# Optimization experiments

Measured on AMD Instinct MI355X. Metric: run time of the kernel, lower is better.

The kernel has to match this reference:

```python
import jax, jax.numpy as jnp
import numpy as np

B, S, N, F_IN = 4, 256, 500, 32
D, L = 64, 2
TEMP = 0.5
EPS = 1e-5

def gelu(x):
    return jax.nn.gelu(x, approximate=False)  # torch default GELU (erf)

def layernorm(h, g, b):
    mu = h.mean(-1, keepdims=True)
    var = ((h - mu) ** 2).mean(-1, keepdims=True)
    return (h - mu) * jax.lax.rsqrt(var + EPS) * g + b

def gru_last(x_seq, Wih, Whh, bih, bhh):
    # x_seq: [B, T, I]; torch nn.GRU gate math, h0 = 0; returns final hidden [B, D]
    xp = jnp.einsum('bti,gi->btg', x_seq, Wih) + bih  # precompute input gates [B, T, 3D]
    d = Whh.shape[1]
    def step(h, xpt):
        gh = h @ Whh.T + bhh
        xr, xz, xn = jnp.split(xpt, 3, axis=-1)
        hr, hz, hn = jnp.split(gh, 3, axis=-1)
        r = jax.nn.sigmoid(xr + hr)
        z = jax.nn.sigmoid(xz + hz)
        n = jnp.tanh(xn + r * hn)
        return (1.0 - z) * n + z * h, None
    h0 = jnp.zeros((x_seq.shape[0], d), x_seq.dtype)
    h, _ = jax.lax.scan(step, h0, xp.transpose(1, 0, 2))
    return h

def forward(x, ip_W, ip_b, from_embed, to_embed, gl_W, gl_b, gl_g, gl_be,
            Wih_s, Whh_s, bih_s, bhh_s, Wih_m, Whh_m, bih_m, bhh_m,
            Wih_l, Whh_l, bih_l, bhh_l, dh_W1, dh_b1, dh_W2, dh_b2):
    # input_proj: Linear + GELU (Dropout is identity in eval)
    x = gelu(jnp.einsum('bsnf,df->bsnd', x, ip_W) + ip_b)  # [B,S,N,D]
    # learned adjacency: softmax over destination nodes
    adj = jax.nn.softmax((from_embed @ to_embed.T) / TEMP, axis=-1)  # [N,N]
    for i in range(gl_W.shape[0]):
        agg = jnp.einsum('bsnd,nm->bsmd', x, adj)
        h = gelu(jnp.einsum('bsnd,ed->bsne', x + agg, gl_W[i]) + gl_b[i])
        x = layernorm(h, gl_g[i], gl_be[i])
    b, s, n, d = x.shape
    x_flat = x.reshape(b, s, n * d)
    h_s = gru_last(x_flat[:, -10:, :], Wih_s, Whh_s, bih_s, bhh_s)
    h_m = gru_last(x_flat[:, -20:, :], Wih_m, Whh_m, bih_m, bhh_m)
    h_l = gru_last(x_flat, Wih_l, Whh_l, bih_l, bhh_l)
    h = jnp.concatenate([h_s, h_m, h_l], axis=-1)  # [B, 3D]
    h = gelu(h @ dh_W1.T + dh_b1)
    return h @ dh_W2.T + dh_b2  # direction logits [B, N]

def setup_inputs():
    key = jax.random.key(0)
    it = iter(jax.random.split(key, 40))
    rn = lambda shape, s=0.02: jax.random.normal(next(it), shape, jnp.float32) * s
    I = N * D
    return {
        'x': jax.random.normal(next(it), (B, S, N, F_IN), jnp.float32),
        'ip_W': rn((D, F_IN)), 'ip_b': jnp.zeros((D,), jnp.float32),
        'from_embed': rn((N, 32), 0.1), 'to_embed': rn((N, 32), 0.1),
        'gl_W': rn((L, D, D)), 'gl_b': jnp.zeros((L, D), jnp.float32),
        'gl_g': jnp.ones((L, D), jnp.float32), 'gl_be': jnp.zeros((L, D), jnp.float32),
        'Wih_s': rn((3 * D, I)), 'Whh_s': rn((3 * D, D)),
        'bih_s': jnp.zeros((3 * D,), jnp.float32), 'bhh_s': jnp.zeros((3 * D,), jnp.float32),
        'Wih_m': rn((3 * D, I)), 'Whh_m': rn((3 * D, D)),
        'bih_m': jnp.zeros((3 * D,), jnp.float32), 'bhh_m': jnp.zeros((3 * D,), jnp.float32),
        'Wih_l': rn((3 * D, I)), 'Whh_l': rn((3 * D, D)),
        'bih_l': jnp.zeros((3 * D,), jnp.float32), 'bhh_l': jnp.zeros((3 * D,), jnp.float32),
        'dh_W1': rn((D, 3 * D)), 'dh_b1': jnp.zeros((D,), jnp.float32),
        'dh_W2': rn((N, D)), 'dh_b2': jnp.zeros((N,), jnp.float32),
    }

def reference(x, ip_W, ip_b, from_embed, to_embed, gl_W, gl_b, gl_g, gl_be,
              Wih_s, Whh_s, bih_s, bhh_s, Wih_m, Whh_m, bih_m, bhh_m,
              Wih_l, Whh_l, bih_l, bhh_l, dh_W1, dh_b1, dh_W2, dh_b2):
    return forward(x, ip_W, ip_b, from_embed, to_embed, gl_W, gl_b, gl_g, gl_be,
                   Wih_s, Whh_s, bih_s, bhh_s, Wih_m, Whh_m, bih_m, bhh_m,
                   Wih_l, Whh_l, bih_l, bhh_l, dh_W1, dh_b1, dh_W2, dh_b2)
```

## Files before the change

### kernel.cpp

```cpp
#include <hip/hip_runtime.h>
#include <math.h>

#define NN 500
#define DD 64
#define NPAD 512
#define COLS 65536
#define BS_TOT 1024
#define I_DIM 32000
#define KS_GRU 40
#define KSL 800

typedef __attribute__((ext_vector_type(8))) short bf16x8;
typedef __attribute__((ext_vector_type(4))) float f32x4;

__device__ __forceinline__ float gelu_f(float x) {
    return 0.5f * x * (1.0f + erff(x * 0.70710678118654752440f));
}

__device__ __forceinline__ unsigned short bf16_rn(float x) {
    unsigned int u = __float_as_uint(x);
    unsigned int r = u + 0x7FFFu + ((u >> 16) & 1u);
    return (unsigned short)(r >> 16);
}
__device__ __forceinline__ float bf16_tof(unsigned short h) {
    return __uint_as_float(((unsigned int)h) << 16);
}
__device__ __forceinline__ unsigned int pack_hl(float x) {
    unsigned short h = bf16_rn(x);
    unsigned short l = bf16_rn(x - bf16_tof(h));
    return (unsigned int)h | ((unsigned int)l << 16);
}
__device__ __forceinline__ float unpack_val(unsigned int u) {
    return __uint_as_float(u << 16) + __uint_as_float(u & 0xFFFF0000u);
}
__device__ __forceinline__ void split4(float4 v, short4& h4, short4& l4) {
    h4.x = (short)bf16_rn(v.x); l4.x = (short)bf16_rn(v.x - bf16_tof((unsigned short)h4.x));
    h4.y = (short)bf16_rn(v.y); l4.y = (short)bf16_rn(v.y - bf16_tof((unsigned short)h4.y));
    h4.z = (short)bf16_rn(v.z); l4.z = (short)bf16_rn(v.z - bf16_tof((unsigned short)h4.z));
    h4.w = (short)bf16_rn(v.w); l4.w = (short)bf16_rn(v.w - bf16_tof((unsigned short)h4.w));
}

__device__ __forceinline__ int frag_off(int row, int q) {
    return ((((row >> 4) * 4 + q) * 16) + (row & 15)) * 16;
}

__global__ __launch_bounds__(512)
void adj_kernel(const float* __restrict__ fe, const float* __restrict__ te,
                short* __restrict__ adjTh, short* __restrict__ adjTl)
{
    __shared__ float fr[32];
    __shared__ float red[8];
    __shared__ float red2[8];
    const int n = blockIdx.x;
    const int tid = threadIdx.x;
    if (tid < 32) fr[tid] = fe[n * 32 + tid];
    __syncthreads();
    const int m = tid;
    float s = -1e30f;
    if (m < NN) {
        float acc = 0.f;
        #pragma unroll
        for (int f = 0; f < 32; ++f) acc += fr[f] * te[m * 32 + f];
        s = acc * 2.0f;
    }
    float v = s;
    #pragma unroll
    for (int off = 32; off; off >>= 1) v = fmaxf(v, __shfl_xor(v, off));
    if ((tid & 63) == 0) red[tid >> 6] = v;
    __syncthreads();
    float bmax = red[0];
    #pragma unroll
    for (int i = 1; i < 8; ++i) bmax = fmaxf(bmax, red[i]);
    float e = (m < NN) ? expf(s - bmax) : 0.f;
    float v2 = e;
    #pragma unroll
    for (int off = 32; off; off >>= 1) v2 += __shfl_xor(v2, off);
    if ((tid & 63) == 0) red2[tid >> 6] = v2;
    __syncthreads();
    float bsum = 0.f;
    #pragma unroll
    for (int i = 0; i < 8; ++i) bsum += red2[i];
    if (m < NN) {
        float p = e / bsum + ((m == n) ? 1.0f : 0.0f);
        unsigned short h = bf16_rn(p);
        adjTh[(size_t)m * NPAD + n] = (short)h;
        adjTl[(size_t)m * NPAD + n] = (short)bf16_rn(p - bf16_tof(h));
    }
}

__global__ __launch_bounds__(256)
void wsplit_kernel(const float* __restrict__ W, short* __restrict__ H,
                   short* __restrict__ L, int n4)
{
    int i = blockIdx.x * 256 + threadIdx.x;
    if (i < n4) {
        float4 v = *(const float4*)&W[i * 4];
        short4 h4, l4;
        split4(v, h4, l4);
        *(short4*)&H[i * 4] = h4;
        *(short4*)&L[i * 4] = l4;
    }
}

__global__ __launch_bounds__(256)
void proj_mfma_kernel(const float* __restrict__ xin,
                      const short* __restrict__ Wh, const short* __restrict__ Wl,
                      const float* __restrict__ ipb, unsigned int* __restrict__ Xhl)
{
    const int tid  = threadIdx.x;
    const int lane = tid & 63;
    const int wave = tid >> 6;
    const int q = lane >> 4, r16 = lane & 15;
    const size_t row0 = (size_t)blockIdx.x * 128 + wave * 32;

    float bB[4];
    #pragma unroll
    for (int ci = 0; ci < 4; ++ci) bB[ci] = ipb[ci * 16 + r16];

    bf16x8 wh[4], wl[4];
    #pragma unroll
    for (int ci = 0; ci < 4; ++ci) {
        int off = (ci * 16 + r16) * 32 + q * 8;
        wh[ci] = *(const bf16x8*)&Wh[off];
        wl[ci] = *(const bf16x8*)&Wl[off];
    }

    f32x4 acc[2][4];
    #pragma unroll
    for (int i = 0; i < 2; ++i)
        #pragma unroll
        for (int j = 0; j < 4; ++j) acc[i][j] = (f32x4){0.f, 0.f, 0.f, 0.f};

    #pragma unroll
    for (int mi = 0; mi < 2; ++mi) {
        const size_t row = row0 + mi * 16 + r16;
        const int n = (int)(row >> 10), bs = (int)(row & 1023);
        const float* src = &xin[((size_t)bs * NN + n) * 32 + q * 8];
        float4 v0 = *(const float4*)src;
        float4 v1 = *(const float4*)(src + 4);
        short4 h0, l0, h1, l1;
        split4(v0, h0, l0);
        split4(v1, h1, l1);
        bf16x8 ah, al;
        ah[0] = h0.x; ah[1] = h0.y; ah[2] = h0.z; ah[3] = h0.w;
        ah[4] = h1.x; ah[5] = h1.y; ah[6] = h1.z; ah[7] = h1.w;
        al[0] = l0.x; al[1] = l0.y; al[2] = l0.z; al[3] = l0.w;
        al[4] = l1.x; al[5] = l1.y; al[6] = l1.z; al[7] = l1.w;
        #pragma unroll
        for (int ci = 0; ci < 4; ++ci) {
            acc[mi][ci] = __builtin_amdgcn_mfma_f32_16x16x32_bf16(ah, wh[ci], acc[mi][ci], 0, 0, 0);
            acc[mi][ci] = __builtin_amdgcn_mfma_f32_16x16x32_bf16(ah, wl[ci], acc[mi][ci], 0, 0, 0);
            acc[mi][ci] = __builtin_amdgcn_mfma_f32_16x16x32_bf16(al, wh[ci], acc[mi][ci], 0, 0, 0);
        }
    }

    #pragma unroll
    for (int mi = 0; mi < 2; ++mi) {
        #pragma unroll
        for (int rg = 0; rg < 4; ++rg) {
            size_t grow = row0 + mi * 16 + q * 4 + rg;
            #pragma unroll
            for (int ci = 0; ci < 4; ++ci) {
                float y = gelu_f(acc[mi][ci][rg] + bB[ci]);
                Xhl[grow * 64 + ci * 16 + r16] = pack_hl(y);
            }
        }
    }
}

__global__ __launch_bounds__(256)
void agg_mfma_kernel(const unsigned int* __restrict__ Xhl,
                     const short* __restrict__ adjTh, const short* __restrict__ adjTl,
                     unsigned int* __restrict__ Yhl)
{
    __shared__ __align__(16) short Ah[2][4096];
    __shared__ __align__(16) short Al[2][4096];
    __shared__ __align__(16) short Bh[2][4096];
    __shared__ __align__(16) short Bl[2][4096];

    const int tid  = threadIdx.x;
    const int lane = tid & 63;
    const int wave = tid >> 6;
    const int wm = (wave >> 1) * 64;
    const int wc = (wave & 1) * 64;
    const int q = lane >> 4, r16 = lane & 15;
    const int m0 = blockIdx.x * 128;
    const int c0 = blockIdx.y * 128;

    const int sa_m = tid >> 1, sa_kh = tid & 1;
    const int sb_c = tid & 127, sb_kh = tid >> 7;
    const size_t cb = (size_t)(c0 + sb_c);

    f32x4 acc[4][4];
    #pragma unroll
    for (int i = 0; i < 4; ++i)
        #pragma unroll
        for (int j = 0; j < 4; ++j) acc[i][j] = (f32x4){0.f, 0.f, 0.f, 0.f};

    {
        const size_t base = (size_t)(m0 + sa_m) * NPAD + sa_kh * 16;
        bf16x8 h0 = *(const bf16x8*)&adjTh[base];
        bf16x8 h1 = *(const bf16x8*)&adjTh[base + 8];
        bf16x8 l0 = *(const bf16x8*)&adjTl[base];
        bf16x8 l1 = *(const bf16x8*)&adjTl[base + 8];
        *(bf16x8*)((char*)Ah[0] + frag_off(sa_m, sa_kh * 2))     = h0;
        *(bf16x8*)((char*)Ah[0] + frag_off(sa_m, sa_kh * 2 + 1)) = h1;
        *(bf16x8*)((char*)Al[0] + frag_off(sa_m, sa_kh * 2))     = l0;
        *(bf16x8*)((char*)Al[0] + frag_off(sa_m, sa_kh * 2 + 1)) = l1;

        unsigned int u[16];
        #pragma unroll
        for (int j = 0; j < 16; ++j) {
            int kk = sb_kh * 16 + j;
            u[j] = (kk < NN) ? Xhl[(size_t)kk * COLS + cb] : 0u;
        }
        bf16x8 bh0, bh1, bl0, bl1;
        #pragma unroll
        for (int j = 0; j < 8; ++j) {
            bh0[j] = (short)(u[j] & 0xFFFFu);     bl0[j] = (short)(u[j] >> 16);
            bh1[j] = (short)(u[8 + j] & 0xFFFFu); bl1[j] = (short)(u[8 + j] >> 16);
        }
        *(bf16x8*)((char*)Bh[0] + frag_off(sb_c, sb_kh * 2))     = bh0;
        *(bf16x8*)((char*)Bh[0] + frag_off(sb_c, sb_kh * 2 + 1)) = bh1;
        *(bf16x8*)((char*)Bl[0] + frag_off(sb_c, sb_kh * 2))     = bl0;
        *(bf16x8*)((char*)Bl[0] + frag_off(sb_c, sb_kh * 2 + 1)) = bl1;
    }
    __syncthreads();

    for (int kc = 0; kc < 16; ++kc) {
        const int cur = kc & 1;
        bf16x8 nAh0, nAh1, nAl0, nAl1;
        unsigned int nu[16];
        if (kc < 15) {
            const int k0n = (kc + 1) * 32;
            const size_t base = (size_t)(m0 + sa_m) * NPAD + k0n + sa_kh * 16;
            nAh0 = *(const bf16x8*)&adjTh[base];
            nAh1 = *(const bf16x8*)&adjTh[base + 8];
            nAl0 = *(const bf16x8*)&adjTl[base];
            nAl1 = *(const bf16x8*)&adjTl[base + 8];
            #pragma unroll
            for (int j = 0; j < 16; ++j) {
                int kk = k0n + sb_kh * 16 + j;
                nu[j] = (kk < NN) ? Xhl[(size_t)kk * COLS + cb] : 0u;
            }
        }
        bf16x8 ah[4], al[4];
        #pragma unroll
        for (int mi = 0; mi < 4; ++mi) {
            int off = frag_off(wm + mi * 16 + r16, q);
            ah[mi] = *(const bf16x8*)((const char*)Ah[cur] + off);
            al[mi] = *(const bf16x8*)((const char*)Al[cur] + off);
        }
        #pragma unroll
        for (int ci = 0; ci < 4; ++ci) {
            int off = frag_off(wc + ci * 16 + r16, q);
            bf16x8 bh = *(const bf16x8*)((const char*)Bh[cur] + off);
            bf16x8 bl = *(const bf16x8*)((const char*)Bl[cur] + off);
            #pragma unroll
            for (int mi = 0; mi < 4; ++mi) {
                acc[mi][ci] = __builtin_amdgcn_mfma_f32_16x16x32_bf16(ah[mi], bh, acc[mi][ci], 0, 0, 0);
                acc[mi][ci] = __builtin_amdgcn_mfma_f32_16x16x32_bf16(ah[mi], bl, acc[mi][ci], 0, 0, 0);
                acc[mi][ci] = __builtin_amdgcn_mfma_f32_16x16x32_bf16(al[mi], bh, acc[mi][ci], 0, 0, 0);
            }
        }
        if (kc < 15) {
            const int nb = cur ^ 1;
            *(bf16x8*)((char*)Ah[nb] + frag_off(sa_m, sa_kh * 2))     = nAh0;
            *(bf16x8*)((char*)Ah[nb] + frag_off(sa_m, sa_kh * 2 + 1)) = nAh1;
            *(bf16x8*)((char*)Al[nb] + frag_off(sa_m, sa_kh * 2))     = nAl0;
            *(bf16x8*)((char*)Al[nb] + frag_off(sa_m, sa_kh * 2 + 1)) = nAl1;
            bf16x8 bh0, bh1, bl0, bl1;
            #pragma unroll
            for (int j = 0; j < 8; ++j) {
                bh0[j] = (short)(nu[j] & 0xFFFFu);     bl0[j] = (short)(nu[j] >> 16);
                bh1[j] = (short)(nu[8 + j] & 0xFFFFu); bl1[j] = (short)(nu[8 + j] >> 16);
            }
            *(bf16x8*)((char*)Bh[nb] + frag_off(sb_c, sb_kh * 2))     = bh0;
            *(bf16x8*)((char*)Bh[nb] + frag_off(sb_c, sb_kh * 2 + 1)) = bh1;
            *(bf16x8*)((char*)Bl[nb] + frag_off(sb_c, sb_kh * 2))     = bl0;
            *(bf16x8*)((char*)Bl[nb] + frag_off(sb_c, sb_kh * 2 + 1)) = bl1;
        }
        __syncthreads();
    }

    #pragma unroll
    for (int mi = 0; mi < 4; ++mi) {
        #pragma unroll
        for (int r = 0; r < 4; ++r) {
            int m = m0 + wm + mi * 16 + q * 4 + r;
            if (m < NN) {
                #pragma unroll
                for (int ci = 0; ci < 4; ++ci) {
                    size_t idx = (size_t)m * COLS + c0 + wc + ci * 16 + r16;
                    Yhl[idx] = pack_hl(acc[mi][ci][r]);
                }
            }
        }
    }
}

__global__ __launch_bounds__(256)
void hln_stream_kernel(unsigned int* __restrict__ Xio,
                       const short* __restrict__ Wh, const short* __restrict__ Wl,
                       const float* __restrict__ glb, const float* __restrict__ glg,
                       const float* __restrict__ glbe)
{
    const int tid  = threadIdx.x;
    const int lane = tid & 63;
    const int wave = tid >> 6;
    const int q = lane >> 4, r16 = lane & 15;
    const size_t row0 = (size_t)blockIdx.x * 128 + wave * 32;

    float bB2[4], bG2[4], bE2[4];
    #pragma unroll
    for (int ci = 0; ci < 4; ++ci) {
        int e = ci * 16 + r16;
        bB2[ci] = glb[e]; bG2[ci] = glg[e]; bE2[ci] = glbe[e];
    }

    f32x4 acc[2][4];
    #pragma unroll
    for (int i = 0; i < 2; ++i)
        #pragma unroll
        for (int j = 0; j < 4; ++j) acc[i][j] = (f32x4){0.f, 0.f, 0.f, 0.f};

    #pragma unroll
    for (int kh = 0; kh < 2; ++kh) {
        bf16x8 wh[4], wl[4];
        #pragma unroll
        for (int ci = 0; ci < 4; ++ci) {
            int off = (ci * 16 + r16) * 64 + kh * 32 + q * 8;
            wh[ci] = *(const bf16x8*)&Wh[off];
            wl[ci] = *(const bf16x8*)&Wl[off];
        }
        #pragma unroll
        for (int mi = 0; mi < 2; ++mi) {
            const size_t row = row0 + mi * 16 + r16;
            const unsigned int* src = &Xio[row * 64 + kh * 32 + q * 8];
            uint4 u0 = *(const uint4*)src;
            uint4 u1 = *(const uint4*)(src + 4);
            bf16x8 ah, al;
            ah[0] = (short)(u0.x & 0xFFFFu); al[0] = (short)(u0.x >> 16);
            ah[1] = (short)(u0.y & 0xFFFFu); al[1] = (short)(u0.y >> 16);
            ah[2] = (short)(u0.z & 0xFFFFu); al[2] = (short)(u0.z >> 16);
            ah[3] = (short)(u0.w & 0xFFFFu); al[3] = (short)(u0.w >> 16);
            ah[4] = (short)(u1.x & 0xFFFFu); al[4] = (short)(u1.x >> 16);
            ah[5] = (short)(u1.y & 0xFFFFu); al[5] = (short)(u1.y >> 16);
            ah[6] = (short)(u1.z & 0xFFFFu); al[6] = (short)(u1.z >> 16);
            ah[7] = (short)(u1.w & 0xFFFFu); al[7] = (short)(u1.w >> 16);
            #pragma unroll
            for (int ci = 0; ci < 4; ++ci) {
                acc[mi][ci] = __builtin_amdgcn_mfma_f32_16x16x32_bf16(ah, wh[ci], acc[mi][ci], 0, 0, 0);
                acc[mi][ci] = __builtin_amdgcn_mfma_f32_16x16x32_bf16(ah, wl[ci], acc[mi][ci], 0, 0, 0);
                acc[mi][ci] = __builtin_amdgcn_mfma_f32_16x16x32_bf16(al, wh[ci], acc[mi][ci], 0, 0, 0);
            }
        }
    }

    #pragma unroll
    for (int mi = 0; mi < 2; ++mi) {
        #pragma unroll
        for (int rg = 0; rg < 4; ++rg) {
            float h[4];
            float s1 = 0.f;
            #pragma unroll
            for (int ci = 0; ci < 4; ++ci) {
                h[ci] = gelu_f(acc[mi][ci][rg] + bB2[ci]);
                s1 += h[ci];
            }
            #pragma unroll
            for (int off = 1; off < 16; off <<= 1) s1 += __shfl_xor(s1, off);
            float mu = s1 * (1.f / 64.f);
            float s2 = 0.f;
            #pragma unroll
            for (int ci = 0; ci < 4; ++ci) { float dc = h[ci] - mu; s2 += dc * dc; }
            #pragma unroll
            for (int off = 1; off < 16; off <<= 1) s2 += __shfl_xor(s2, off);
            float rs = 1.f / sqrtf(s2 * (1.f / 64.f) + 1e-5f);
            size_t grow = row0 + mi * 16 + q * 4 + rg;
            #pragma unroll
            for (int ci = 0; ci < 4; ++ci) {
                float y = (h[ci] - mu) * rs * bG2[ci] + bE2[ci];
                Xio[grow * 64 + ci * 16 + r16] = pack_hl(y);
            }
        }
    }
}

__global__ __launch_bounds__(256)
void wconv_kernel(const float* __restrict__ W0, const float* __restrict__ W1,
                  const float* __restrict__ W2,
                  short* __restrict__ h0, short* __restrict__ l0,
                  short* __restrict__ h1, short* __restrict__ l1,
                  short* __restrict__ h2, short* __restrict__ l2)
{
    const int gi = blockIdx.y;
    const float* W = (gi == 0) ? W0 : (gi == 1) ? W1 : W2;
    short* H = (gi == 0) ? h0 : (gi == 1) ? h1 : h2;
    short* L = (gi == 0) ? l0 : (gi == 1) ? l1 : l2;
    const size_t i = ((size_t)blockIdx.x * 256 + threadIdx.x) * 4;
    float4 v = *(const float4*)&W[i];
    short4 h4, l4;
    split4(v, h4, l4);
    *(short4*)&H[i] = h4;
    *(short4*)&L[i] = l4;
}

__global__ __launch_bounds__(256)
void gru_pre_mfma_kernel(const unsigned int* __restrict__ Xhl,
                         const short* __restrict__ Wh0, const short* __restrict__ Wl0,
                         const short* __restrict__ Wh1, const short* __restrict__ Wl1,
                         const short* __restrict__ Wh2, const short* __restrict__ Wl2,
                         float* __restrict__ p0, float* __restrict__ p1,
                         float* __restrict__ p2)
{
    __shared__ __align__(16) short Ah[2048];
    __shared__ __align__(16) short Al[2048];
    __shared__ __align__(16) short Bh[6144];
    __shared__ __align__(16) short Bl[6144];

    const int bid = blockIdx.x;
    int gi, mtid, ks;
    if (bid < 40)       { gi = 0; mtid = 0;             ks = bid; }
    else if (bid < 120) { int r = bid - 40;  gi = 1; ks = r % 40; mtid = r / 40; }
    else                { int r = bid - 120; gi = 2; ks = r % 40; mtid = r / 40; }
    const short* Wh = (gi == 0) ? Wh0 : (gi == 1) ? Wh1 : Wh2;
    const short* Wl = (gi == 0) ? Wl0 : (gi == 1) ? Wl1 : Wl2;
    float* partial  = (gi == 0) ? p0 : (gi == 1) ? p1 : p2;
    const int Trows = (gi == 0) ? 10 : (gi == 1) ? 20 : 256;
    const int toff  = (gi == 0) ? 246 : (gi == 1) ? 236 : 0;
    const int M     = (gi == 0) ? 40 : (gi == 1) ? 80 : 1024;
    const int R0 = mtid * 64;

    const int tid  = threadIdx.x;
    const int lane = tid & 63;
    const int wave = tid >> 6;
    const int wr = (wave & 1) * 32;
    const int wg = (wave >> 1) * 96;
    const int q = lane >> 4, r16 = lane & 15;

    const int sa_r = tid >> 2, sa_kq = tid & 3;
    const bool vldA = (R0 + sa_r < M);
    int btA = 0;
    if (vldA) { int R = R0 + sa_r; int b = R / Trows, t = R - b * Trows; btA = b * 256 + toff + t; }

    f32x4 acc[2][6];
    #pragma unroll
    for (int i = 0; i < 2; ++i)
        #pragma unroll
        for (int j = 0; j < 6; ++j) acc[i][j] = (f32x4){0.f, 0.f, 0.f, 0.f};

    for (int c = 0; c < KSL / 32; ++c) {
        const int k0 = ks * KSL + c * 32;
        {
            const int kk = k0 + sa_kq * 8;
            const int nn = kk >> 6, d0 = kk & 63;
            uint4 u0 = make_uint4(0u, 0u, 0u, 0u), u1 = u0;
            if (vldA) {
                const unsigned int* src = &Xhl[((size_t)nn * BS_TOT + btA) * 64 + d0];
                u0 = *(const uint4*)src;
                u1 = *(const uint4*)(src + 4);
            }
            short4 h0 = make_short4((short)(u0.x & 0xFFFF), (short)(u0.y & 0xFFFF),
                                    (short)(u0.z & 0xFFFF), (short)(u0.w & 0xFFFF));
            short4 l0 = make_short4((short)(u0.x >> 16), (short)(u0.y >> 16),
                                    (short)(u0.z >> 16), (short)(u0.w >> 16));
            short4 h1 = make_short4((short)(u1.x & 0xFFFF), (short)(u1.y & 0xFFFF),
                                    (short)(u1.z & 0xFFFF), (short)(u1.w & 0xFFFF));
            short4 l1 = make_short4((short)(u1.x >> 16), (short)(u1.y >> 16),
                                    (short)(u1.z >> 16), (short)(u1.w >> 16));
            const int fo = frag_off(sa_r, sa_kq);
            *(short4*)((char*)Ah + fo)     = h0;
            *(short4*)((char*)Ah + fo + 8) = h1;
            *(short4*)((char*)Al + fo)     = l0;
            *(short4*)((char*)Al + fo + 8) = l1;
        }
        #pragma unroll
        for (int l = 0; l < 3; ++l) {
            int idx = tid + l * 256;
            int g = idx >> 2, kq = idx & 3;
            const size_t src = (size_t)g * I_DIM + k0 + kq * 8;
            bf16x8 hv = *(const bf16x8*)&Wh[src];
            bf16x8 lv = *(const bf16x8*)&Wl[src];
            const int fo = frag_off(g, kq);
            *(bf16x8*)((char*)Bh + fo) = hv;
            *(bf16x8*)((char*)Bl + fo) = lv;
        }
        __syncthreads();
        bf16x8 ah[2], al[2];
        #pragma unroll
        for (int mi = 0; mi < 2; ++mi) {
            const int fo = frag_off(wr + mi * 16 + r16, q);
            ah[mi] = *(const bf16x8*)((const char*)Ah + fo);
            al[mi] = *(const bf16x8*)((const char*)Al + fo);
        }
        #pragma unroll
        for (int ci = 0; ci < 6; ++ci) {
            const int fo = frag_off(wg + ci * 16 + r16, q);
            bf16x8 bh = *(const bf16x8*)((const char*)Bh + fo);
            bf16x8 bl = *(const bf16x8*)((const char*)Bl + fo);
            #pragma unroll
            for (int mi = 0; mi < 2; ++mi) {
                acc[mi][ci] = __builtin_amdgcn_mfma_f32_16x16x32_bf16(ah[mi], bh, acc[mi][ci], 0, 0, 0);
                acc[mi][ci] = __builtin_amdgcn_mfma_f32_16x16x32_bf16(ah[mi], bl, acc[mi][ci], 0, 0, 0);
                acc[mi][ci] = __builtin_amdgcn_mfma_f32_16x16x32_bf16(al[mi], bh, acc[mi][ci], 0, 0, 0);
            }
        }
        __syncthreads();
    }
    #pragma unroll
    for (int mi = 0; mi < 2; ++mi) {
        #pragma unroll
        for (int r = 0; r < 4; ++r) {
            int R = R0 + wr + mi * 16 + q * 4 + r;
            if (R < M) {
                #pragma unroll
                for (int ci = 0; ci < 6; ++ci)
                    partial[((size_t)ks * M + R) * 192 + wg + ci * 16 + r16] = acc[mi][ci][r];
            }
        }
    }
}

__global__ __launch_bounds__(192)
void gru_reduce_fused_kernel(const float* __restrict__ p0, const float* __restrict__ p1,
                             const float* __restrict__ p2,
                             const float* __restrict__ bih0, const float* __restrict__ bih1,
                             const float* __restrict__ bih2,
                             float* __restrict__ xp0, float* __restrict__ xp1,
                             float* __restrict__ xp2)
{
    int r = blockIdx.x;
    const float* partial; const float* bih; float* xp; int M;
    if (r < 40)       { partial = p0; bih = bih0; xp = xp0; M = 40; }
    else if (r < 120) { r -= 40;  partial = p1; bih = bih1; xp = xp1; M = 80; }
    else              { r -= 120; partial = p2; bih = bih2; xp = xp2; M = 1024; }
    const int g = threadIdx.x;
    float acc = bih[g];
    for (int ks = 0; ks < KS_GRU; ++ks)
        acc += partial[((size_t)ks * M + r) * 192 + g];
    xp[(size_t)r * 192 + g] = acc;
}

__global__ __launch_bounds__(192)
void gru_scan_kernel(const float* __restrict__ xp_s, const float* __restrict__ xp_m,
                     const float* __restrict__ xp_l,
                     const float* __restrict__ Whh_s, const float* __restrict__ Whh_m,
                     const float* __restrict__ Whh_l,
                     const float* __restrict__ bhh_s, const float* __restrict__ bhh_m,
                     const float* __restrict__ bhh_l,
                     float* __restrict__ hcat)
{
    __shared__ float h[64];
    __shared__ float gh[192];
    const int blk = blockIdx.x;
    const int g3 = blk >> 2, b = blk & 3;
    const float* xp  = (g3 == 0) ? xp_s : (g3 == 1) ? xp_m : xp_l;
    const float* Whh = (g3 == 0) ? Whh_s : (g3 == 1) ? Whh_m : Whh_l;
    const float* bhh = (g3 == 0) ? bhh_s : (g3 == 1) ? bhh_m : bhh_l;
    const int T = (g3 == 0) ? 10 : (g3 == 1) ? 20 : 256;
    const int g = threadIdx.x;

    float w[64];
    #pragma unroll
    for (int k4 = 0; k4 < 16; ++k4) {
        float4 v = *(const float4*)&Whh[g * 64 + k4 * 4];
        w[k4 * 4 + 0] = v.x; w[k4 * 4 + 1] = v.y;
        w[k4 * 4 + 2] = v.z; w[k4 * 4 + 3] = v.w;
    }
    const float bh = bhh[g];
    if (g < 64) h[g] = 0.f;

    const float* xpb = xp + (size_t)b * T * 192;
    float xr_c = 0.f, xz_c = 0.f, xn_c = 0.f;
    if (g < 64) { xr_c = xpb[g]; xz_c = xpb[64 + g]; xn_c = xpb[128 + g]; }
    __syncthreads();

    for (int t = 0; t < T; ++t) {
        float xr_n = 0.f, xz_n = 0.f, xn_n = 0.f;
        if (t + 1 < T && g < 64) {
            const float* xq = xpb + (size_t)(t + 1) * 192;
            xr_n = xq[g]; xz_n = xq[64 + g]; xn_n = xq[128 + g];
        }
        float a0 = 0.f, a1 = 0.f, a2 = 0.f, a3 = 0.f;
        #pragma unroll
        for (int k4 = 0; k4 < 16; ++k4) {
            float4 hv = ((const float4*)h)[k4];
            a0 += hv.x * w[k4 * 4 + 0];
            a1 += hv.y * w[k4 * 4 + 1];
            a2 += hv.z * w[k4 * 4 + 2];
            a3 += hv.w * w[k4 * 4 + 3];
        }
        gh[g] = bh + ((a0 + a1) + (a2 + a3));
        __syncthreads();
        if (g < 64) {
            float hr = gh[g], hz = gh[64 + g], hn = gh[128 + g];
            float r = 1.f / (1.f + __expf(-(xr_c + hr)));
            float z = 1.f / (1.f + __expf(-(xz_c + hz)));
            float pre = xn_c + r * hn;
            float e2 = __expf(2.f * pre);
            float nv = 1.f - 2.f / (e2 + 1.f);
            h[g] = (1.f - z) * nv + z * h[g];
        }
        __syncthreads();
        xr_c = xr_n; xz_c = xz_n; xn_c = xn_n;
    }
    if (g < 64) hcat[b * 192 + g3 * 64 + g] = h[g];
}

__global__ __launch_bounds__(512)
void head_kernel(const float* __restrict__ hcat,
                 const float* __restrict__ W1, const float* __restrict__ b1,
                 const float* __restrict__ W2, const float* __restrict__ b2,
                 float* __restrict__ out)
{
    __shared__ float hc[4][192];
    __shared__ float h1[4][64];
    const int tid = threadIdx.x;
    for (int i = tid; i < 768; i += 512) hc[i / 192][i % 192] = hcat[i];
    __syncthreads();
    if (tid < 256) {
        int b = tid >> 6, e = tid & 63;
        float acc = b1[e];
        #pragma unroll
        for (int k = 0; k < 192; ++k) acc += hc[b][k] * W1[e * 192 + k];
        h1[b][e] = gelu_f(acc);
    }
    __syncthreads();
    for (int o = tid; o < 2000; o += 512) {
        int b = o / 500, n = o % 500;
        float acc = b2[n];
        #pragma unroll
        for (int k = 0; k < 64; ++k) acc += h1[b][k] * W2[n * 64 + k];
        out[o] = acc;
    }
}

extern "C" void kernel_launch(void* const* d_in, const int* in_sizes, int n_in,
                              void* d_out, int out_size, void* d_ws, size_t ws_size,
                              hipStream_t stream)
{
    (void)in_sizes; (void)n_in; (void)out_size; (void)ws_size;
    const float* x    = (const float*)d_in[0];
    const float* ipW  = (const float*)d_in[1];
    const float* ipb  = (const float*)d_in[2];
    const float* fe   = (const float*)d_in[3];
    const float* te   = (const float*)d_in[4];
    const float* glW  = (const float*)d_in[5];
    const float* glb  = (const float*)d_in[6];
    const float* glg  = (const float*)d_in[7];
    const float* glbe = (const float*)d_in[8];
    const float* Wih[3] = {(const float*)d_in[9],  (const float*)d_in[13], (const float*)d_in[17]};
    const float* Whh[3] = {(const float*)d_in[10], (const float*)d_in[14], (const float*)d_in[18]};
    const float* bih[3] = {(const float*)d_in[11], (const float*)d_in[15], (const float*)d_in[19]};
    const float* bhh[3] = {(const float*)d_in[12], (const float*)d_in[16], (const float*)d_in[20]};
    const float* W1 = (const float*)d_in[21];
    const float* b1 = (const float*)d_in[22];
    const float* W2 = (const float*)d_in[23];
    const float* b2 = (const float*)d_in[24];
    float* out = (float*)d_out;

    unsigned int* Xhl = (unsigned int*)d_ws;
    unsigned int* Yhl = Xhl + 32768000;
    short* adjTh = (short*)(Yhl + 32768000);
    short* adjTl = adjTh + NPAD * NPAD;
    short* glWh  = adjTl + NPAD * NPAD;
    short* glWl  = glWh + 8192;
    short* ipWh  = glWl + 8192;
    short* ipWl  = ipWh + 2048;
    short* wbase = (short*)Yhl;
    short* Wh0 = wbase;
    short* Wl0 = Wh0 + 6144000;
    short* Wh1 = Wl0 + 6144000;
    short* Wl1 = Wh1 + 6144000;
    short* Wh2 = Wl1 + 6144000;
    short* Wl2 = Wh2 + 6144000;
    float* pbase = (float*)Yhl + 18432000;
    float* part0 = pbase;
    float* part1 = part0 + 307200;
    float* part2 = part1 + 614400;
    float* xp0   = part2 + 7864320;
    float* xp1   = xp0 + 7680;
    float* xp2   = xp1 + 15360;
    float* hcat  = xp2 + 196608;

    hipMemsetAsync(adjTh, 0, (size_t)NPAD * NPAD * 2 * sizeof(short), stream);
    adj_kernel<<<NN, 512, 0, stream>>>(fe, te, adjTh, adjTl);
    wsplit_kernel<<<8, 256, 0, stream>>>(glW, glWh, glWl, 2048);
    wsplit_kernel<<<2, 256, 0, stream>>>(ipW, ipWh, ipWl, 512);
    proj_mfma_kernel<<<4000, 256, 0, stream>>>(x, ipWh, ipWl, ipb, Xhl);

    agg_mfma_kernel<<<dim3(4, 512), 256, 0, stream>>>(Xhl, adjTh, adjTl, Yhl);
    hln_stream_kernel<<<4000, 256, 0, stream>>>(Yhl, glWh, glWl, glb, glg, glbe);
    agg_mfma_kernel<<<dim3(4, 512), 256, 0, stream>>>(Yhl, adjTh, adjTl, Xhl);
    hln_stream_kernel<<<4000, 256, 0, stream>>>(Xhl, glWh + 4096, glWl + 4096,
                                                glb + 64, glg + 64, glbe + 64);

    wconv_kernel<<<dim3(6000, 3), 256, 0, stream>>>(Wih[0], Wih[1], Wih[2],
                                                    Wh0, Wl0, Wh1, Wl1, Wh2, Wl2);
    gru_pre_mfma_kernel<<<760, 256, 0, stream>>>(Xhl, Wh0, Wl0, Wh1, Wl1, Wh2, Wl2,
                                                 part0, part1, part2);
    gru_reduce_fused_kernel<<<1144, 192, 0, stream>>>(part0, part1, part2,
                                                      bih[0], bih[1], bih[2],
                                                      xp0, xp1, xp2);
    gru_scan_kernel<<<12, 192, 0, stream>>>(xp0, xp1, xp2,
                                            Whh[0], Whh[1], Whh[2],
                                            bhh[0], bhh[1], bhh[2], hcat);
    head_kernel<<<1, 512, 0, stream>>>(hcat, W1, b1, W2, b2, out);
}
```

Measured before the change: 732.7 us.

## Run GRU recurrence with split-bf16 MFMA, batching all four sequences per block

The GRU scan is rewritten so that one block per GRU handles all four batch rows. Each step computes the h·Whh product with bf16x3 split MFMA instructions, with the weights pre-split by extra wsplit launches and kept in registers. A double-buffered hidden state in shared memory cuts each timestep to one barrier instead of two. The goal is to shorten the serial 256-step critical path, at the cost of extra split-precision MFMA work and three small extra kernel launches.

```diff
diff --git a/kernel.cpp b/kernel.cpp
--- a/kernel.cpp
+++ b/kernel.cpp
@@ -542,70 +542,118 @@
     xp[(size_t)r * 192 + g] = acc;
 }
 
-__global__ __launch_bounds__(192)
+__global__ __launch_bounds__(256)
 void gru_scan_kernel(const float* __restrict__ xp_s, const float* __restrict__ xp_m,
                      const float* __restrict__ xp_l,
-                     const float* __restrict__ Whh_s, const float* __restrict__ Whh_m,
-                     const float* __restrict__ Whh_l,
+                     const short* __restrict__ WhS, const short* __restrict__ WlS,
+                     const short* __restrict__ WhM, const short* __restrict__ WlM,
+                     const short* __restrict__ WhL, const short* __restrict__ WlL,
                      const float* __restrict__ bhh_s, const float* __restrict__ bhh_m,
                      const float* __restrict__ bhh_l,
                      float* __restrict__ hcat)
 {
-    __shared__ float h[64];
-    __shared__ float gh[192];
-    const int blk = blockIdx.x;
-    const int g3 = blk >> 2, b = blk & 3;
+    __shared__ float Hs[2][16][68];
+    const int g3 = blockIdx.x;
     const float* xp  = (g3 == 0) ? xp_s : (g3 == 1) ? xp_m : xp_l;
-    const float* Whh = (g3 == 0) ? Whh_s : (g3 == 1) ? Whh_m : Whh_l;
+    const short* Wh  = (g3 == 0) ? WhS : (g3 == 1) ? WhM : WhL;
+    const short* Wl  = (g3 == 0) ? WlS : (g3 == 1) ? WlM : WlL;
     const float* bhh = (g3 == 0) ? bhh_s : (g3 == 1) ? bhh_m : bhh_l;
     const int T = (g3 == 0) ? 10 : (g3 == 1) ? 20 : 256;
-    const int g = threadIdx.x;
-
-    float w[64];
-    #pragma unroll
-    for (int k4 = 0; k4 < 16; ++k4) {
-        float4 v = *(const float4*)&Whh[g * 64 + k4 * 4];
-        w[k4 * 4 + 0] = v.x; w[k4 * 4 + 1] = v.y;
-        w[k4 * 4 + 2] = v.z; w[k4 * 4 + 3] = v.w;
-    }
-    const float bh = bhh[g];
-    if (g < 64) h[g] = 0.f;
-
-    const float* xpb = xp + (size_t)b * T * 192;
-    float xr_c = 0.f, xz_c = 0.f, xn_c = 0.f;
-    if (g < 64) { xr_c = xpb[g]; xz_c = xpb[64 + g]; xn_c = xpb[128 + g]; }
+    const int tid = threadIdx.x, lane = tid & 63, wave = tid >> 6;
+    const int q = lane >> 4, r16 = lane & 15;
+
+    bf16x8 wbh[3][2], wbl[3][2];
+    #pragma unroll
+    for (int tI = 0; tI < 3; ++tI) {
+        const int n = tI * 64 + wave * 16 + r16;
+        #pragma unroll
+        for (int kh = 0; kh < 2; ++kh) {
+            const int off = n * 64 + kh * 32 + q * 8;
+            wbh[tI][kh] = *(const bf16x8*)&Wh[off];
+            wbl[tI][kh] = *(const bf16x8*)&Wl[off];
+        }
+    }
+
+    const bool act = (lane < 16);
+    const int g = wave * 16 + r16;
+    float bhr = 0.f, bhz = 0.f, bhn = 0.f;
+    if (act) { bhr = bhh[g]; bhz = bhh[64 + g]; bhn = bhh[128 + g]; }
+
+    for (int i = tid; i < 2 * 16 * 68; i += 256) ((float*)Hs)[i] = 0.f;
+
+    float hb[4] = {0.f, 0.f, 0.f, 0.f};
+    float xr[4] = {0,0,0,0}, xz[4] = {0,0,0,0}, xn[4] = {0,0,0,0};
+    if (act) {
+        #pragma unroll
+        for (int b = 0; b < 4; ++b) {
+            const float* p = xp + ((size_t)b * T) * 192;
+            xr[b] = p[g]; xz[b] = p[64 + g]; xn[b] = p[128 + g];
+        }
+    }
     __syncthreads();
 
     for (int t = 0; t < T; ++t) {
-        float xr_n = 0.f, xz_n = 0.f, xn_n = 0.f;
-        if (t + 1 < T && g < 64) {
-            const float* xq = xpb + (size_t)(t + 1) * 192;
-            xr_n = xq[g]; xz_n = xq[64 + g]; xn_n = xq[128 + g];
-        }
-        float a0 = 0.f, a1 = 0.f, a2 = 0.f, a3 = 0.f;
-        #pragma unroll
-        for (int k4 = 0; k4 < 16; ++k4) {
-            float4 hv = ((const float4*)h)[k4];
-            a0 += hv.x * w[k4 * 4 + 0];
-            a1 += hv.y * w[k4 * 4 + 1];
-            a2 += hv.z * w[k4 * 4 + 2];
-            a3 += hv.w * w[k4 * 4 + 3];
-        }
-        gh[g] = bh + ((a0 + a1) + (a2 + a3));
+        const int cur = t & 1, nxt = cur ^ 1;
+        float nxr[4] = {0,0,0,0}, nxz[4] = {0,0,0,0}, nxn[4] = {0,0,0,0};
+        if (act && t + 1 < T) {
+            #pragma unroll
+            for (int b = 0; b < 4; ++b) {
+                const float* p = xp + ((size_t)b * T + t + 1) * 192;
+                nxr[b] = p[g]; nxz[b] = p[64 + g]; nxn[b] = p[128 + g];
+            }
+        }
+        bf16x8 ah[2], al[2];
+        #pragma unroll
+        for (int kh = 0; kh < 2; ++kh) {
+            const float* hp = &Hs[cur][r16][kh * 32 + q * 8];
+            float4 v0 = *(const float4*)hp;
+            float4 v1 = *(const float4*)(hp + 4);
+            short4 h0_, l0_, h1_, l1_;
+            split4(v0, h0_, l0_);
+            split4(v1, h1_, l1_);
+            bf16x8 a, b_;
+            a[0] = h0_.x; a[1] = h0_.y; a[2] = h0_.z; a[3] = h0_.w;
+            a[4] = h1_.x; a[5] = h1_.y; a[6] = h1_.z; a[7] = h1_.w;
+            b_[0] = l0_.x; b_[1] = l0_.y; b_[2] = l0_.z; b_[3] = l0_.w;
+            b_[4] = l1_.x; b_[5] = l1_.y; b_[6] = l1_.z; b_[7] = l1_.w;
+            ah[kh] = a; al[kh] = b_;
+        }
+        f32x4 acc0 = (f32x4){0.f,0.f,0.f,0.f};
+        f32x4 acc1 = (f32x4){0.f,0.f,0.f,0.f};
+        f32x4 acc2 = (f32x4){0.f,0.f,0.f,0.f};
+        #pragma unroll
+        for (int kh = 0; kh < 2; ++kh) {
+            acc0 = __builtin_amdgcn_mfma_f32_16x16x32_bf16(ah[kh], wbh[0][kh], acc0, 0, 0, 0);
+            acc0 = __builtin_amdgcn_mfma_f32_16x16x32_bf16(ah[kh], wbl[0][kh], acc0, 0, 0, 0);
+            acc0 = __builtin_amdgcn_mfma_f32_16x16x32_bf16(al[kh], wbh[0][kh], acc0, 0, 0, 0);
+            acc1 = __builtin_amdgcn_mfma_f32_16x16x32_bf16(ah[kh], wbh[1][kh], acc1, 0, 0, 0);
+            acc1 = __builtin_amdgcn_mfma_f32_16x16x32_bf16(ah[kh], wbl[1][kh], acc1, 0, 0, 0);
+            acc1 = __builtin_amdgcn_mfma_f32_16x16x32_bf16(al[kh], wbh[1][kh], acc1, 0, 0, 0);
+            acc2 = __builtin_amdgcn_mfma_f32_16x16x32_bf16(ah[kh], wbh[2][kh], acc2, 0, 0, 0);
+            acc2 = __builtin_amdgcn_mfma_f32_16x16x32_bf16(ah[kh], wbl[2][kh], acc2, 0, 0, 0);
+            acc2 = __builtin_amdgcn_mfma_f32_16x16x32_bf16(al[kh], wbh[2][kh], acc2, 0, 0, 0);
+        }
+        if (act) {
+            #pragma unroll
+            for (int b = 0; b < 4; ++b) {
+                float r = 1.f / (1.f + __expf(-(xr[b] + acc0[b] + bhr)));
+                float z = 1.f / (1.f + __expf(-(xz[b] + acc1[b] + bhz)));
+                float pre = xn[b] + r * (acc2[b] + bhn);
+                float e2 = __expf(2.f * pre);
+                float nv = 1.f - 2.f / (e2 + 1.f);
+                hb[b] = (1.f - z) * nv + z * hb[b];
+                Hs[nxt][b][g] = hb[b];
+            }
+        }
+        #pragma unroll
+        for (int b = 0; b < 4; ++b) { xr[b] = nxr[b]; xz[b] = nxz[b]; xn[b] = nxn[b]; }
         __syncthreads();
-        if (g < 64) {
-            float hr = gh[g], hz = gh[64 + g], hn = gh[128 + g];
-            float r = 1.f / (1.f + __expf(-(xr_c + hr)));
-            float z = 1.f / (1.f + __expf(-(xz_c + hz)));
-            float pre = xn_c + r * hn;
-            float e2 = __expf(2.f * pre);
-            float nv = 1.f - 2.f / (e2 + 1.f);
-            h[g] = (1.f - z) * nv + z * h[g];
-        }
-        __syncthreads();
-        xr_c = xr_n; xz_c = xz_n; xn_c = xn_n;
-    }
-    if (g < 64) hcat[b * 192 + g3 * 64 + g] = h[g];
+    }
+    if (act) {
+        #pragma unroll
+        for (int b = 0; b < 4; ++b)
+            hcat[b * 192 + g3 * 64 + g] = hb[b];
+    }
 }
 
 __global__ __launch_bounds__(512)
@@ -668,6 +716,12 @@
     short* glWl  = glWh + 8192;
     short* ipWh  = glWl + 8192;
     short* ipWl  = ipWh + 2048;
+    short* whhH0 = ipWl + 2048;
+    short* whhL0 = whhH0 + 12288;
+    short* whhH1 = whhL0 + 12288;
+    short* whhL1 = whhH1 + 12288;
+    short* whhH2 = whhL1 + 12288;
+    short* whhL2 = whhH2 + 12288;
     short* wbase = (short*)Yhl;
     short* Wh0 = wbase;
     short* Wl0 = Wh0 + 6144000;
@@ -688,6 +742,9 @@
     adj_kernel<<<NN, 512, 0, stream>>>(fe, te, adjTh, adjTl);
     wsplit_kernel<<<8, 256, 0, stream>>>(glW, glWh, glWl, 2048);
     wsplit_kernel<<<2, 256, 0, stream>>>(ipW, ipWh, ipWl, 512);
+    wsplit_kernel<<<12, 256, 0, stream>>>(Whh[0], whhH0, whhL0, 3072);
+    wsplit_kernel<<<12, 256, 0, stream>>>(Whh[1], whhH1, whhL1, 3072);
+    wsplit_kernel<<<12, 256, 0, stream>>>(Whh[2], whhH2, whhL2, 3072);
     proj_mfma_kernel<<<4000, 256, 0, stream>>>(x, ipWh, ipWl, ipb, Xhl);
 
     agg_mfma_kernel<<<dim3(4, 512), 256, 0, stream>>>(Xhl, adjTh, adjTl, Yhl);
@@ -703,8 +760,8 @@
     gru_reduce_fused_kernel<<<1144, 192, 0, stream>>>(part0, part1, part2,
                                                       bih[0], bih[1], bih[2],
                                                       xp0, xp1, xp2);
-    gru_scan_kernel<<<12, 192, 0, stream>>>(xp0, xp1, xp2,
-                                            Whh[0], Whh[1], Whh[2],
-                                            bhh[0], bhh[1], bhh[2], hcat);
+    gru_scan_kernel<<<3, 256, 0, stream>>>(xp0, xp1, xp2,
+                                           whhH0, whhL0, whhH1, whhL1, whhH2, whhL2,
+                                           bhh[0], bhh[1], bhh[2], hcat);
     head_kernel<<<1, 512, 0, stream>>>(hcat, W1, b1, W2, b2, out);
 }
```

Result: slower. 887.0 us (+21.1%).
